# Performance work log

Hardware: AMD Instinct MI355X
Metric: run time of the kernel (lower is better)

The kernel has to match this reference:

```python
import jax, jax.numpy as jnp
import numpy as np

SLOPE = 0.01  # torch LeakyReLU default negative_slope

def _leaky(v):
    return jnp.where(v >= 0, v, SLOPE * v)

def _conv3d(x, w, b, stride):
    y = jax.lax.conv_general_dilated(
        x, w, window_strides=(stride, stride, stride), padding='VALID',
        dimension_numbers=('NCDHW', 'OIDHW', 'NCDHW'))
    return y + b[None, :, None, None, None]

def setup_inputs() -> dict:
    key = jax.random.key(0)
    ks = jax.random.split(key, 12)
    s = 0.05  # small init scale to keep exp(L1) numerically sane
    x = jax.random.normal(ks[0], (64, 1, 92, 92, 92), dtype=jnp.float32)
    w1 = jax.random.normal(ks[1], (16, 1, 6, 6, 6), dtype=jnp.float32) * s
    b1 = jnp.zeros((16,), jnp.float32)
    w2 = jax.random.normal(ks[2], (32, 16, 5, 5, 5), dtype=jnp.float32) * s
    b2 = jnp.zeros((32,), jnp.float32)
    w3 = jax.random.normal(ks[3], (48, 32, 5, 5, 5), dtype=jnp.float32) * s
    b3 = jnp.zeros((48,), jnp.float32)
    w4 = jax.random.normal(ks[4], (64, 48, 3, 3, 3), dtype=jnp.float32) * s
    b4 = jnp.zeros((64,), jnp.float32)
    T = jax.random.normal(ks[5], (512, 64 * 16), dtype=jnp.float32) * s
    Wm = jax.random.normal(ks[6], (512 + 64, 1), dtype=jnp.float32) * s
    bm = jnp.zeros((1,), jnp.float32)
    return {'x': x, 'w1': w1, 'b1': b1, 'w2': w2, 'b2': b2, 'w3': w3,
            'b3': b3, 'w4': w4, 'b4': b4, 'T': T, 'Wm': Wm, 'bm': bm}

def reference(x, w1, b1, w2, b2, w3, b3, w4, b4, T, Wm, bm):
    h = _leaky(_conv3d(x, w1, b1, 2))   # [N,16,44,44,44]
    h = _leaky(_conv3d(h, w2, b2, 3))   # [N,32,14,14,14]
    h = _leaky(_conv3d(h, w3, b3, 3))   # [N,48,4,4,4]
    h = _leaky(_conv3d(h, w4, b4, 1))   # [N,64,2,2,2]
    feature = h.reshape(h.shape[0], -1)  # [N,512]
    # minibatch discrimination: M [N,64,16]
    M = (feature @ T).reshape(-1, 64, 16)
    # pairwise L1 over last dim -> [N,N,64]; sum_j exp(.) -> [N,64]
    dist = jnp.sum(jnp.abs(M[:, None, :, :] - M[None, :, :, :]), axis=-1)
    out_T = jnp.sum(jnp.exp(dist), axis=1)
    z = jnp.concatenate([feature, out_T], axis=1) @ Wm + bm
    return jax.nn.sigmoid(z)
```

## Files before the change

### kernel.cpp

```cpp
#include <hip/hip_runtime.h>
#include <hip/hip_bf16.h>
#include <hip/hip_fp16.h>

typedef _Float16 v2h __attribute__((ext_vector_type(2)));
typedef _Float16 v8h __attribute__((ext_vector_type(8)));
typedef __fp16  v2hf __attribute__((ext_vector_type(2)));
typedef float v4f __attribute__((ext_vector_type(4)));

static inline __device__ float leaky(float v) { return v >= 0.f ? v : 0.01f * v; }

static inline __device__ v2h pkrtz(float a, float b) {
    v2hf r = __builtin_amdgcn_cvt_pkrtz(a, b);
    return __builtin_bit_cast(v2h, r);
}

#define W4T_OFF   0
#define H3P_OFF   82944
#define H3_OFF    1655808
#define FEAT_OFF  1852416
#define M_OFF     1885184
#define OT_OFF    1950720
#define F16_BASE  1954816
#define WL1_OFF   0
#define BF2_OFF   4608
#define BF3_OFF   81408
#define H2C_OFF   273408
#define H1C_OFF   5893120

__global__ void prep_kernel(const float* __restrict__ w1, const float* __restrict__ w2,
                            const float* __restrict__ w3, const float* __restrict__ w4,
                            float* __restrict__ w4t, _Float16* __restrict__ Bw1,
                            _Float16* __restrict__ Bf2, _Float16* __restrict__ Bf3) {
    int i = blockIdx.x * 256 + threadIdx.x;
    if (i < 4608) {
        int ks = i >> 9, l = (i >> 3) & 63, j = i & 7;
        int oc = l & 15, kg = l >> 4;
        int g = ks * 4 + kg;
        int kz = g / 6, ky = g % 6;
        Bw1[i] = (j < 6) ? (_Float16)w1[oc * 216 + kz * 36 + ky * 6 + j]
                         : (_Float16)0.f;
    } else if (i < 4608 + 76800) {
        int j2 = i - 4608;
        int nt = j2 / 38400, r = j2 % 38400;
        int t = r / 512, l = (r % 512) >> 3, j = r & 7;
        int oc = nt * 16 + (l & 15);
        int k = (l >> 4) * 8 + j;
        int kz = t / 15, ky = (t % 15) / 3, kxp = t % 3;
        int kx = kxp * 2 + (k >= 16 ? 1 : 0);
        int ic = k & 15;
        Bf2[j2] = (kx < 5) ? (_Float16)w2[oc * 2000 + ic * 125 + kz * 25 + ky * 5 + kx]
                           : (_Float16)0.f;
    } else if (i < 4608 + 76800 + 192000) {
        int j3 = i - (4608 + 76800);
        int nt = j3 / 64000, r = j3 % 64000;
        int tap = r / 512, l = (r % 512) >> 3, j = r & 7;
        int oc = nt * 16 + (l & 15);
        int ic = (l >> 4) * 8 + j;
        Bf3[j3] = (_Float16)w3[oc * 4000 + ic * 125 + tap];
    } else {
        int j4 = i - (4608 + 76800 + 192000);
        if (j4 < 82944) {
            int oc = j4 & 63, t = j4 >> 6;
            w4t[j4] = w4[oc * 1296 + t];
        }
    }
}

__global__ __launch_bounds__(256) void conv1_kernel(
    const float* __restrict__ x, const _Float16* __restrict__ Bw1,
    const float* __restrict__ b1, _Float16* __restrict__ h1c, int n0) {
    __shared__ __align__(16) _Float16 tile[144 * 96];
    int tid = threadIdx.x;
    int b = blockIdx.x;
    int nb = b / 121, rr = b % 121;
    int zq = rr / 11, yt = rr % 11;
    const float* xin = x + (long)(n0 + nb) * 778688;
    int izb = 8 * zq, iyb = 8 * yt;

    for (int u = tid; u < 3312; u += 256) {
        int row = u / 23, c = u % 23;
        int iz = izb + row / 12, iy = iyb + row % 12;
        const float4 v = *(const float4*)(xin + (long)iz * 8464 + iy * 92 + 4 * c);
        union { v2h h[2]; uint2 u2; } pk;
        pk.h[0] = pkrtz(v.x, v.y);
        pk.h[1] = pkrtz(v.z, v.w);
        *(uint2*)(tile + row * 96 + 4 * c) = pk.u2;
    }
    if (tid < 144) {
        uint2 zz; zz.x = 0u; zz.y = 0u;
        *(uint2*)(tile + tid * 96 + 92) = zz;
    }
    __syncthreads();

    int lane = tid & 63, wv = tid >> 6;
    int col = lane & 15, kg = lane >> 4;

    v8h Bv[9];
#pragma unroll
    for (int ks = 0; ks < 9; ks++) Bv[ks] = *(const v8h*)(Bw1 + ks * 512 + lane * 8);

    int offs[9];
#pragma unroll
    for (int ks = 0; ks < 9; ks++) {
        int g = ks * 4 + kg;
        int kz = g / 6, ky = g % 6;
        offs[ks] = (kz * 12 + ky) * 192;
    }
    float bias = b1[col];
    const uint* lds32 = (const uint*)tile;

    int z = zq * 4 + wv;
    for (int yy = 0; yy < 4; yy++) {
#pragma unroll
        for (int xt = 0; xt < 3; xt++) {
            int xo_base = (xt == 2) ? 28 : (xt << 4);
            int base_byte = (24 * wv + 2 * yy) * 192 + (xo_base + col) * 4;
            v4f acc = {0.f, 0.f, 0.f, 0.f};
#pragma unroll
            for (int ks = 0; ks < 9; ks++) {
                int di = (base_byte + offs[ks]) >> 2;
                union { uint u[4]; v8h h; } A;
                A.u[0] = lds32[di + 0];
                A.u[1] = lds32[di + 1];
                A.u[2] = lds32[di + 2];
                A.u[3] = lds32[di + 3];
                acc = __builtin_amdgcn_mfma_f32_16x16x32_f16(A.h, Bv[ks], acc, 0, 0, 0);
            }
            int y = yt * 4 + yy;
            long obase = ((long)((nb * 44 + z) * 44 + y) * 44 + xo_base + kg * 4) * 16 + col;
#pragma unroll
            for (int reg = 0; reg < 4; reg++) {
                h1c[obase + reg * 16] = (_Float16)leaky(acc[reg] + bias);
            }
        }
    }
}

__global__ __launch_bounds__(256) void conv2_kernel(
    const _Float16* __restrict__ h1c, const _Float16* __restrict__ Bf2,
    const float* __restrict__ b2, _Float16* __restrict__ h2c, int n0, int mlimit) {
    int tid = threadIdx.x;
    int lane = tid & 63, wv = tid >> 6;
    int nwg = gridDim.x;
    int orig = blockIdx.x;
    int xcd = orig & 7, lid = orig >> 3;
    int q = nwg >> 3, r = nwg & 7;
    int swz = (xcd < r ? xcd * (q + 1) : r * (q + 1) + (xcd - r) * q) + lid;
    int t0 = (swz * 4 + wv) * 4;
    int col = lane & 15, kgrp = lane >> 4;
    int par = kgrp >> 1, ico = (kgrp & 1) * 8;

    int base[4];
    bool valid[4];
#pragma unroll
    for (int i = 0; i < 4; i++) {
        int m = (t0 + i) * 16 + col;
        valid[i] = m < mlimit;
        int mm = valid[i] ? m : 0;
        int nl = mm / 2744, rm = mm % 2744;
        int z = rm / 196; rm %= 196;
        int y = rm / 14, xx = rm % 14;
        base[i] = nl * 1362944 + z * 3 * 30976 + y * 3 * 704 + xx * 3 * 16 + ico + par * 16;
    }

    v4f acc[4][2];
#pragma unroll
    for (int i = 0; i < 4; i++)
#pragma unroll
        for (int nt = 0; nt < 2; nt++) acc[i][nt] = (v4f){0.f, 0.f, 0.f, 0.f};

    int t = 0;
    for (int kz = 0; kz < 5; kz++) {
        for (int ky = 0; ky < 5; ky++) {
#pragma unroll
            for (int kxp = 0; kxp < 3; kxp++, t++) {
                int d = kz * 30976 + ky * 704 + kxp * 32;
                v8h B0 = *(const v8h*)(Bf2 + t * 512 + lane * 8);
                v8h B1 = *(const v8h*)(Bf2 + (75 + t) * 512 + lane * 8);
                v8h A0 = *(const v8h*)(h1c + base[0] + d);
                v8h A1 = *(const v8h*)(h1c + base[1] + d);
                v8h A2 = *(const v8h*)(h1c + base[2] + d);
                v8h A3 = *(const v8h*)(h1c + base[3] + d);
                acc[0][0] = __builtin_amdgcn_mfma_f32_16x16x32_f16(A0, B0, acc[0][0], 0, 0, 0);
                acc[0][1] = __builtin_amdgcn_mfma_f32_16x16x32_f16(A0, B1, acc[0][1], 0, 0, 0);
                acc[1][0] = __builtin_amdgcn_mfma_f32_16x16x32_f16(A1, B0, acc[1][0], 0, 0, 0);
                acc[1][1] = __builtin_amdgcn_mfma_f32_16x16x32_f16(A1, B1, acc[1][1], 0, 0, 0);
                acc[2][0] = __builtin_amdgcn_mfma_f32_16x16x32_f16(A2, B0, acc[2][0], 0, 0, 0);
                acc[2][1] = __builtin_amdgcn_mfma_f32_16x16x32_f16(A2, B1, acc[2][1], 0, 0, 0);
                acc[3][0] = __builtin_amdgcn_mfma_f32_16x16x32_f16(A3, B0, acc[3][0], 0, 0, 0);
                acc[3][1] = __builtin_amdgcn_mfma_f32_16x16x32_f16(A3, B1, acc[3][1], 0, 0, 0);
            }
        }
    }

#pragma unroll
    for (int i = 0; i < 4; i++) {
        if (!valid[i]) continue;
#pragma unroll
        for (int nt = 0; nt < 2; nt++) {
            int oc = nt * 16 + col;
            float bb = b2[oc];
#pragma unroll
            for (int reg = 0; reg < 4; reg++) {
                int mlocal = (t0 + i) * 16 + kgrp * 4 + reg;
                float vv = leaky(acc[i][nt][reg] + bb);
                h2c[(long)(n0 * 2744 + mlocal) * 32 + oc] = (_Float16)vv;
            }
        }
    }
}

__global__ __launch_bounds__(256) void conv3_kernel(
    const _Float16* __restrict__ h2c, const _Float16* __restrict__ Bf3,
    const float* __restrict__ b3, float* __restrict__ h3) {
    __shared__ float part[3][64][13];
    int tid = threadIdx.x;
    int lane = tid & 63, wv = tid >> 6;
    int mt = blockIdx.x;
    int col = lane & 15, kgrp = lane >> 4;
    int m = mt * 16 + col;
    int n = m >> 6, pos = m & 63;
    int z = pos >> 4, y = (pos >> 2) & 3, xx = pos & 3;
    int base = (n * 2744 + z * 3 * 196 + y * 3 * 14 + xx * 3) * 32 + kgrp * 8;

    v4f acc[3];
#pragma unroll
    for (int nt = 0; nt < 3; nt++) acc[nt] = (v4f){0.f, 0.f, 0.f, 0.f};

    int tap0 = wv * 32;
    int tap1 = tap0 + 32 < 125 ? tap0 + 32 : 125;
    for (int tap = tap0; tap < tap1; tap++) {
        int kz = tap / 25, rr = tap % 25, ky = rr / 5, kx = rr % 5;
        int d = (kz * 196 + ky * 14 + kx) * 32;
        v8h A  = *(const v8h*)(h2c + base + d);
        v8h B0 = *(const v8h*)(Bf3 + tap * 512 + lane * 8);
        v8h B1 = *(const v8h*)(Bf3 + (125 + tap) * 512 + lane * 8);
        v8h B2 = *(const v8h*)(Bf3 + (250 + tap) * 512 + lane * 8);
        acc[0] = __builtin_amdgcn_mfma_f32_16x16x32_f16(A, B0, acc[0], 0, 0, 0);
        acc[1] = __builtin_amdgcn_mfma_f32_16x16x32_f16(A, B1, acc[1], 0, 0, 0);
        acc[2] = __builtin_amdgcn_mfma_f32_16x16x32_f16(A, B2, acc[2], 0, 0, 0);
    }

    if (wv > 0) {
#pragma unroll
        for (int nt = 0; nt < 3; nt++)
#pragma unroll
            for (int reg = 0; reg < 4; reg++)
                part[wv - 1][lane][nt * 4 + reg] = acc[nt][reg];
    }
    __syncthreads();
    if (wv == 0) {
#pragma unroll
        for (int w = 0; w < 3; w++)
#pragma unroll
            for (int nt = 0; nt < 3; nt++)
#pragma unroll
                for (int reg = 0; reg < 4; reg++)
                    acc[nt][reg] += part[w][lane][nt * 4 + reg];
#pragma unroll
        for (int nt = 0; nt < 3; nt++) {
            int oc = nt * 16 + col;
            float bb = b3[oc];
#pragma unroll
            for (int reg = 0; reg < 4; reg++) {
                int md = mt * 16 + kgrp * 4 + reg;
                h3[((md >> 6) * 48 + oc) * 64 + (md & 63)] = leaky(acc[nt][reg] + bb);
            }
        }
    }
}

__global__ void conv4_kernel(const float* __restrict__ h3, const float* __restrict__ w4t,
                             const float* __restrict__ b4, float* __restrict__ feat) {
    int o = blockIdx.x * 128 + threadIdx.x;
    int pos = o & 7;
    int oc  = (o >> 3) & 63;
    int n   = o >> 9;
    int px = pos & 1, py = (pos >> 1) & 1, pz = pos >> 2;
    const float* xn = h3 + (long)n * 48 * 64;
    float acc = 0.f;
    for (int ic = 0; ic < 48; ic++) {
        const float* xc = xn + ic * 64;
        int tb = ic * 27;
#pragma unroll
        for (int kz = 0; kz < 3; kz++)
#pragma unroll
            for (int ky = 0; ky < 3; ky++)
#pragma unroll
                for (int kx = 0; kx < 3; kx++) {
                    float v = xc[(pz + kz) * 16 + (py + ky) * 4 + (px + kx)];
                    acc += v * w4t[(tb + (kz * 3 + ky) * 3 + kx) * 64 + oc];
                }
    }
    feat[o] = leaky(acc + b4[oc]);
}

__global__ void m_kernel(const float* __restrict__ feat, const float* __restrict__ T,
                         float* __restrict__ M) {
    int o = blockIdx.x * 256 + threadIdx.x;
    int col = o & 1023;
    int n   = o >> 10;
    const float* fr = feat + n * 512;
    float acc = 0.f;
#pragma unroll 4
    for (int f = 0; f < 512; f++) acc += fr[f] * T[f * 1024 + col];
    M[o] = acc;
}

__global__ void outt_kernel(const float* __restrict__ M, float* __restrict__ oT) {
    __shared__ float part[3][64];
    int i = blockIdx.x;
    int tid = threadIdx.x;
    int k = tid & 63, jq = tid >> 6;
    float mi[16];
    const float4* Mi = (const float4*)(M + i * 1024 + k * 16);
#pragma unroll
    for (int q = 0; q < 4; q++) {
        float4 a = Mi[q];
        mi[q*4+0] = a.x; mi[q*4+1] = a.y; mi[q*4+2] = a.z; mi[q*4+3] = a.w;
    }
    float s = 0.f;
    for (int j = jq * 16; j < jq * 16 + 16; j++) {
        const float4* Mj = (const float4*)(M + j * 1024 + k * 16);
        float d = 0.f;
#pragma unroll
        for (int q = 0; q < 4; q++) {
            float4 a = Mj[q];
            d += fabsf(mi[q*4+0]-a.x) + fabsf(mi[q*4+1]-a.y) + fabsf(mi[q*4+2]-a.z) + fabsf(mi[q*4+3]-a.w);
        }
        s += __expf(d);
    }
    if (jq > 0) part[jq - 1][k] = s;
    __syncthreads();
    if (jq == 0) {
        s += part[0][k] + part[1][k] + part[2][k];
        oT[i * 64 + k] = s;
    }
}

__global__ void final_kernel(const float* __restrict__ feat, const float* __restrict__ oT,
                             const float* __restrict__ Wm, const float* __restrict__ bm,
                             float* __restrict__ out) {
    int i = blockIdx.x;
    int lane = threadIdx.x;
    const float* fr = feat + i * 512;
    float z = 0.f;
#pragma unroll
    for (int q = 0; q < 8; q++) z += fr[lane + q * 64] * Wm[lane + q * 64];
    z += oT[i * 64 + lane] * Wm[512 + lane];
#pragma unroll
    for (int off = 32; off > 0; off >>= 1) z += __shfl_down(z, off);
    if (lane == 0) out[i] = 1.f / (1.f + __expf(-(z + bm[0])));
}

extern "C" void kernel_launch(void* const* d_in, const int* in_sizes, int n_in,
                              void* d_out, int out_size, void* d_ws, size_t ws_size,
                              hipStream_t stream) {
    const float* x  = (const float*)d_in[0];
    const float* w1 = (const float*)d_in[1];
    const float* b1 = (const float*)d_in[2];
    const float* w2 = (const float*)d_in[3];
    const float* b2 = (const float*)d_in[4];
    const float* w3 = (const float*)d_in[5];
    const float* b3 = (const float*)d_in[6];
    const float* w4 = (const float*)d_in[7];
    const float* b4 = (const float*)d_in[8];
    const float* T  = (const float*)d_in[9];
    const float* Wm = (const float*)d_in[10];
    const float* bm = (const float*)d_in[11];

    float* ws   = (float*)d_ws;
    float* w4t  = ws + W4T_OFF;
    float* h3   = ws + H3_OFF;
    float* feat = ws + FEAT_OFF;
    float* Mb   = ws + M_OFF;
    float* oT   = ws + OT_OFF;
    _Float16* f16b = (_Float16*)(ws + F16_BASE);
    _Float16* Bw1  = f16b + WL1_OFF;
    _Float16* Bf2  = f16b + BF2_OFF;
    _Float16* Bf3  = f16b + BF3_OFF;
    _Float16* h2c  = f16b + H2C_OFF;
    _Float16* h1c  = f16b + H1C_OFF;

    prep_kernel<<<1392, 256, 0, stream>>>(w1, w2, w3, w4, w4t, Bw1, Bf2, Bf3);

    size_t fixed_bytes = (size_t)F16_BASE * 4 + (size_t)H1C_OFF * 2;
    int NB;
    if (ws_size >= fixed_bytes + (64ll * 1362944 + 64) * 2) NB = 64;
    else if (ws_size >= fixed_bytes + (16ll * 1362944 + 64) * 2) NB = 16;
    else NB = 8;

    for (int n0 = 0; n0 < 64; n0 += NB) {
        conv1_kernel<<<NB * 121, 256, 0, stream>>>(x, Bw1, b1, h1c, n0);
        int mlimit = NB * 2744;
        int blocks2 = (mlimit + 255) / 256;
        conv2_kernel<<<blocks2, 256, 0, stream>>>(h1c, Bf2, b2, h2c, n0, mlimit);
    }
    conv3_kernel<<<256, 256, 0, stream>>>(h2c, Bf3, b3, h3);
    conv4_kernel<<<256, 128, 0, stream>>>(h3, w4t, b4, feat);
    m_kernel<<<256, 256, 0, stream>>>(feat, T, Mb);
    outt_kernel<<<64, 256, 0, stream>>>(Mb, oT);
    final_kernel<<<64, 64, 0, stream>>>(feat, oT, Wm, bm, (float*)d_out);
}
```

Baseline: 612.7 us.

## Make conv1 persistent with double-buffered LDS prefetch of input tiles

Turns conv1 into a persistent kernel with a fixed grid of 512 blocks that loop over tiles. Each iteration loads the next tile's input into registers while the MFMA work runs on the current LDS buffer, then converts it to fp16 and writes it into the other buffer. The aim is to hide global-load latency behind compute. The cost is twice the LDS (about 54KB per block), launch bounds set for two blocks per CU, and more register pressure from 13 float4 prefetch registers.

Result: faster. 582.6 us (-4.9%).

```diff
diff --git a/kernel.cpp b/kernel.cpp
--- a/kernel.cpp
+++ b/kernel.cpp
@@ -15,7 +15,6 @@
 }
 
 #define W4T_OFF   0
-#define H3P_OFF   82944
 #define H3_OFF    1655808
 #define FEAT_OFF  1852416
 #define M_OFF     1885184
@@ -66,73 +65,119 @@
     }
 }
 
-__global__ __launch_bounds__(256) void conv1_kernel(
+__global__ __launch_bounds__(256, 2) void conv1_kernel(
     const float* __restrict__ x, const _Float16* __restrict__ Bw1,
-    const float* __restrict__ b1, _Float16* __restrict__ h1c, int n0) {
-    __shared__ __align__(16) _Float16 tile[144 * 96];
+    const float* __restrict__ b1, _Float16* __restrict__ h1c, int n0, int NT) {
+    __shared__ __align__(16) _Float16 buf[2][13824];
     int tid = threadIdx.x;
-    int b = blockIdx.x;
-    int nb = b / 121, rr = b % 121;
-    int zq = rr / 11, yt = rr % 11;
-    const float* xin = x + (long)(n0 + nb) * 778688;
-    int izb = 8 * zq, iyb = 8 * yt;
-
-    for (int u = tid; u < 3312; u += 256) {
-        int row = u / 23, c = u % 23;
-        int iz = izb + row / 12, iy = iyb + row % 12;
-        const float4 v = *(const float4*)(xin + (long)iz * 8464 + iy * 92 + 4 * c);
-        union { v2h h[2]; uint2 u2; } pk;
-        pk.h[0] = pkrtz(v.x, v.y);
-        pk.h[1] = pkrtz(v.z, v.w);
-        *(uint2*)(tile + row * 96 + 4 * c) = pk.u2;
-    }
+    int lane = tid & 63, wv = tid >> 6;
+    int col = lane & 15, kg = lane >> 4;
+
+    int t0 = blockIdx.x;
+    if (t0 >= NT) return;
+
+    int D_[13], W_[13];
+    bool act_[13];
+#pragma unroll
+    for (int i = 0; i < 13; i++) {
+        int u = tid + i * 256;
+        act_[i] = (u < 3312);
+        int uu = act_[i] ? u : 0;
+        int row = uu / 23, c = uu % 23;
+        D_[i] = (row / 12) * 8464 + (row % 12) * 92 + 4 * c;
+        W_[i] = row * 96 + 4 * c;
+    }
+
+    v8h Bv[9];
+#pragma unroll
+    for (int ks = 0; ks < 9; ks++) Bv[ks] = *(const v8h*)(Bw1 + ks * 512 + lane * 8);
+    int offs[9];
+#pragma unroll
+    for (int ks = 0; ks < 9; ks++) {
+        int g = ks * 4 + kg;
+        offs[ks] = ((g / 6) * 12 + (g % 6)) * 192;
+    }
+    float bias = b1[col];
+
     if (tid < 144) {
         uint2 zz; zz.x = 0u; zz.y = 0u;
-        *(uint2*)(tile + tid * 96 + 92) = zz;
+        *(uint2*)(&buf[0][tid * 96 + 92]) = zz;
+        *(uint2*)(&buf[1][tid * 96 + 92]) = zz;
+    }
+
+    {
+        int nb = t0 / 121, rr = t0 % 121;
+        const float* bp = x + (long)(n0 + nb) * 778688 + (rr / 11) * 8 * 8464 + (rr % 11) * 8 * 92;
+        float4 ld[13];
+#pragma unroll
+        for (int i = 0; i < 13; i++) if (act_[i]) ld[i] = *(const float4*)(bp + D_[i]);
+#pragma unroll
+        for (int i = 0; i < 13; i++) if (act_[i]) {
+            union { v2h h[2]; uint2 u2; } pk;
+            pk.h[0] = pkrtz(ld[i].x, ld[i].y);
+            pk.h[1] = pkrtz(ld[i].z, ld[i].w);
+            *(uint2*)(&buf[0][W_[i]]) = pk.u2;
+        }
     }
     __syncthreads();
 
-    int lane = tid & 63, wv = tid >> 6;
-    int col = lane & 15, kg = lane >> 4;
-
-    v8h Bv[9];
-#pragma unroll
-    for (int ks = 0; ks < 9; ks++) Bv[ks] = *(const v8h*)(Bw1 + ks * 512 + lane * 8);
-
-    int offs[9];
-#pragma unroll
-    for (int ks = 0; ks < 9; ks++) {
-        int g = ks * 4 + kg;
-        int kz = g / 6, ky = g % 6;
-        offs[ks] = (kz * 12 + ky) * 192;
-    }
-    float bias = b1[col];
-    const uint* lds32 = (const uint*)tile;
-
-    int z = zq * 4 + wv;
-    for (int yy = 0; yy < 4; yy++) {
-#pragma unroll
-        for (int xt = 0; xt < 3; xt++) {
-            int xo_base = (xt == 2) ? 28 : (xt << 4);
-            int base_byte = (24 * wv + 2 * yy) * 192 + (xo_base + col) * 4;
-            v4f acc = {0.f, 0.f, 0.f, 0.f};
-#pragma unroll
-            for (int ks = 0; ks < 9; ks++) {
-                int di = (base_byte + offs[ks]) >> 2;
-                union { uint u[4]; v8h h; } A;
-                A.u[0] = lds32[di + 0];
-                A.u[1] = lds32[di + 1];
-                A.u[2] = lds32[di + 2];
-                A.u[3] = lds32[di + 3];
-                acc = __builtin_amdgcn_mfma_f32_16x16x32_f16(A.h, Bv[ks], acc, 0, 0, 0);
+    int cur = 0;
+    int stride = gridDim.x;
+    for (int t = t0; t < NT; t += stride) {
+        int tn = t + stride;
+        bool hn = tn < NT;
+        float4 ld[13];
+        if (hn) {
+            int nb = tn / 121, rr = tn % 121;
+            const float* bp = x + (long)(n0 + nb) * 778688 + (rr / 11) * 8 * 8464 + (rr % 11) * 8 * 92;
+#pragma unroll
+            for (int i = 0; i < 13; i++) if (act_[i]) ld[i] = *(const float4*)(bp + D_[i]);
+        }
+        __builtin_amdgcn_sched_barrier(0);
+
+        {
+            int nb = t / 121, rr = t % 121;
+            int zq = rr / 11, yt = rr % 11;
+            const uint* lds32 = (const uint*)&buf[cur][0];
+            int z = zq * 4 + wv;
+            for (int yy = 0; yy < 4; yy++) {
+#pragma unroll
+                for (int xt = 0; xt < 3; xt++) {
+                    int xo_base = (xt == 2) ? 28 : (xt << 4);
+                    int base_byte = (24 * wv + 2 * yy) * 192 + (xo_base + col) * 4;
+                    v4f acc = {0.f, 0.f, 0.f, 0.f};
+#pragma unroll
+                    for (int ks = 0; ks < 9; ks++) {
+                        int di = (base_byte + offs[ks]) >> 2;
+                        union { uint u[4]; v8h h; } A;
+                        A.u[0] = lds32[di + 0];
+                        A.u[1] = lds32[di + 1];
+                        A.u[2] = lds32[di + 2];
+                        A.u[3] = lds32[di + 3];
+                        acc = __builtin_amdgcn_mfma_f32_16x16x32_f16(A.h, Bv[ks], acc, 0, 0, 0);
+                    }
+                    int y = yt * 4 + yy;
+                    long obase = ((long)((nb * 44 + z) * 44 + y) * 44 + xo_base + kg * 4) * 16 + col;
+#pragma unroll
+                    for (int reg = 0; reg < 4; reg++) {
+                        h1c[obase + reg * 16] = (_Float16)leaky(acc[reg] + bias);
+                    }
+                }
             }
-            int y = yt * 4 + yy;
-            long obase = ((long)((nb * 44 + z) * 44 + y) * 44 + xo_base + kg * 4) * 16 + col;
-#pragma unroll
-            for (int reg = 0; reg < 4; reg++) {
-                h1c[obase + reg * 16] = (_Float16)leaky(acc[reg] + bias);
+        }
+
+        if (hn) {
+            _Float16* wb = &buf[cur ^ 1][0];
+#pragma unroll
+            for (int i = 0; i < 13; i++) if (act_[i]) {
+                union { v2h h[2]; uint2 u2; } pk;
+                pk.h[0] = pkrtz(ld[i].x, ld[i].y);
+                pk.h[1] = pkrtz(ld[i].z, ld[i].w);
+                *(uint2*)(wb + W_[i]) = pk.u2;
             }
         }
+        __syncthreads();
+        cur ^= 1;
     }
 }
 
@@ -391,7 +436,7 @@
     else NB = 8;
 
     for (int n0 = 0; n0 < 64; n0 += NB) {
-        conv1_kernel<<<NB * 121, 256, 0, stream>>>(x, Bw1, b1, h1c, n0);
+        conv1_kernel<<<512, 256, 0, stream>>>(x, Bw1, b1, h1c, n0, NB * 121);
         int mlimit = NB * 2744;
         int blocks2 = (mlimit + 255) / 256;
         conv2_kernel<<<blocks2, 256, 0, stream>>>(h1c, Bf2, b2, h2c, n0, mlimit);
```
